# Performance work log

Hardware: AMD Instinct MI355X
Metric: run time of the kernel (lower is better)

## Reference

```python
import jax, jax.numpy as jnp
import numpy as np


def setup_inputs() -> dict:
    key = jax.random.key(0)
    inputs = jax.random.normal(key, (32, 56, 56, 256), dtype=jnp.float32)
    return {"inputs": inputs, "n": 48}


def reference(inputs, n):
    # Flatten per batch row: [B, H*W*C]
    B = inputs.shape[0]
    flat = inputs.reshape(B, -1)
    # k-th largest value per row is the threshold
    values, _ = jax.lax.top_k(flat, n)
    thresholds = values[:, -1].reshape(B, 1, 1, 1)
    mask = (inputs >= thresholds).astype(inputs.dtype)
    return inputs * mask
```

## Files before the change

### kernel.cpp

```cpp
#include <hip/hip_runtime.h>
#include <stdint.h>

#define ROWS 32
#define ROW_LEN 802816
#define ROW_LEN4 200704
#define BPR 98
#define F4_PER_BLOCK 2048
#define THREADS 256
#define F4_PER_THREAD 8
#define TG 3.0f
#define BCAP 40
#define CAP_ROW (BPR * BCAP)
#define SLOTS_PT 16

#define OFF_BCNT 501760
#define OFF_THR  514304

__device__ __forceinline__ uint32_t fkey(float x) {
    uint32_t u = __float_as_uint(x);
    return (u & 0x80000000u) ? ~u : (u | 0x80000000u);
}
__device__ __forceinline__ float fkey_inv(uint32_t k) {
    uint32_t u = (k & 0x80000000u) ? (k & 0x7FFFFFFFu) : ~k;
    return __uint_as_float(u);
}

__global__ __launch_bounds__(THREADS) void k_spec(const float* __restrict__ in,
                                                  uint32_t* __restrict__ cand,
                                                  int* __restrict__ bcnt) {
    __shared__ uint32_t lc[BCAP];
    __shared__ int lcnt;
    const int row = blockIdx.x / BPR;
    const int blk = blockIdx.x % BPR;
    if (threadIdx.x == 0) lcnt = 0;
    __syncthreads();
    const float4* p = (const float4*)in + (size_t)row * ROW_LEN4
                      + (size_t)blk * F4_PER_BLOCK + threadIdx.x;
#pragma unroll
    for (int v = 0; v < F4_PER_THREAD; ++v) {
        float4 d = p[v * THREADS];
        if (d.x > TG) { int q = atomicAdd(&lcnt, 1); if (q < BCAP) lc[q] = fkey(d.x); }
        if (d.y > TG) { int q = atomicAdd(&lcnt, 1); if (q < BCAP) lc[q] = fkey(d.y); }
        if (d.z > TG) { int q = atomicAdd(&lcnt, 1); if (q < BCAP) lc[q] = fkey(d.z); }
        if (d.w > TG) { int q = atomicAdd(&lcnt, 1); if (q < BCAP) lc[q] = fkey(d.w); }
    }
    __syncthreads();
    const int c = lcnt;
    if (threadIdx.x == 0) bcnt[row * BPR + blk] = c;
    const int cc = c < BCAP ? c : BCAP;
    for (int i = threadIdx.x; i < cc; i += THREADS)
        cand[((size_t)row * BPR + blk) * BCAP + i] = lc[i];
}

__device__ __forceinline__ void pick_digit(uint32_t* h, int t, int r,
                                           int* sh_sel, int* sh_rank) {
#pragma unroll
    for (int off = 1; off < 256; off <<= 1) {
        uint32_t v = h[t] + ((t + off < 256) ? h[t + off] : 0u);
        __syncthreads();
        h[t] = v;
        __syncthreads();
    }
    const uint32_t Sd = h[t];
    const uint32_t Sd1 = (t < 255) ? h[t + 1] : 0u;
    if ((int)Sd >= r && (int)Sd1 < r) { *sh_sel = t; *sh_rank = r - (int)Sd1; }
    __syncthreads();
}

__global__ __launch_bounds__(THREADS) void k_sel(const float* __restrict__ in,
                                                 const int* __restrict__ n_ptr,
                                                 const int* __restrict__ bcnt,
                                                 const uint32_t* __restrict__ cand,
                                                 float* __restrict__ thr) {
    __shared__ int lb[BPR];
    __shared__ uint32_t h[256];
    __shared__ int sh_sel, sh_rank, sh_m, sh_bad;
    const int row = blockIdx.x;
    const int t = threadIdx.x;
    const int n = *n_ptr;

    if (t == 0) { sh_m = 0; sh_bad = 0; }
    __syncthreads();
    {
        int lsum = 0, lbad = 0;
        for (int b = t; b < BPR; b += THREADS) {
            const int c = bcnt[row * BPR + b];
            lbad |= (c > BCAP);
            const int cc = c < BCAP ? c : BCAP;
            lb[b] = cc;
            lsum += cc;
        }
        if (lsum) atomicAdd(&sh_m, lsum);
        if (lbad) atomicOr(&sh_bad, 1);
    }
    __syncthreads();
    const int m = sh_m;
    const bool ok = (!sh_bad) && (m >= n) && (n >= 1);

    if (ok) {
        uint32_t key[SLOTS_PT];
        bool val[SLOTS_PT];
#pragma unroll
        for (int j = 0; j < SLOTS_PT; ++j) {
            const int slot = j * THREADS + t;
            uint32_t k = 0; bool v = false;
            if (slot < CAP_ROW) {
                k = cand[(size_t)row * CAP_ROW + slot];
                const int b = slot / BCAP;
                v = (slot - b * BCAP) < lb[b];
            }
            key[j] = k; val[j] = v;
        }
        uint32_t prefix = 0, msk = 0;
        int r = n;
        for (int rd = 0; rd < 4; ++rd) {
            const int shn = 24 - rd * 8;
            h[t] = 0;
            __syncthreads();
#pragma unroll
            for (int j = 0; j < SLOTS_PT; ++j)
                if (val[j] && (key[j] & msk) == prefix)
                    atomicAdd(&h[(key[j] >> shn) & 255u], 1u);
            __syncthreads();
            pick_digit(h, t, r, &sh_sel, &sh_rank);
            prefix |= ((uint32_t)sh_sel) << shn;
            msk |= 255u << shn;
            r = sh_rank;
            __syncthreads();
        }
        if (t == 0) thr[row] = fkey_inv(prefix);
    } else {
        uint32_t prefix = 0, msk = 0;
        int r = (n < 1) ? 1 : n;
        const float4* p = (const float4*)in + (size_t)row * ROW_LEN4;
        for (int rd = 0; rd < 4; ++rd) {
            const int shn = 24 - rd * 8;
            h[t] = 0;
            __syncthreads();
            for (int i = t; i < ROW_LEN4; i += THREADS) {
                const float4 d = p[i];
                uint32_t k;
                k = fkey(d.x); if ((k & msk) == prefix) atomicAdd(&h[(k >> shn) & 255u], 1u);
                k = fkey(d.y); if ((k & msk) == prefix) atomicAdd(&h[(k >> shn) & 255u], 1u);
                k = fkey(d.z); if ((k & msk) == prefix) atomicAdd(&h[(k >> shn) & 255u], 1u);
                k = fkey(d.w); if ((k & msk) == prefix) atomicAdd(&h[(k >> shn) & 255u], 1u);
            }
            __syncthreads();
            pick_digit(h, t, r, &sh_sel, &sh_rank);
            prefix |= ((uint32_t)sh_sel) << shn;
            msk |= 255u << shn;
            r = sh_rank;
            __syncthreads();
        }
        if (t == 0) thr[row] = fkey_inv(prefix);
    }
}

__global__ __launch_bounds__(THREADS) void k_mask(const float* __restrict__ in,
                                                  const float* __restrict__ thr,
                                                  float* __restrict__ out) {
    const int row = blockIdx.x / BPR;
    const int blk = blockIdx.x % BPR;
    const float t = thr[row];
    const size_t base = (size_t)row * ROW_LEN4 + (size_t)blk * F4_PER_BLOCK + threadIdx.x;
    const float4* p = (const float4*)in + base;
    float4* q = (float4*)out + base;
#pragma unroll
    for (int v = 0; v < F4_PER_THREAD; ++v) {
        float4 d = p[v * THREADS];
        d.x = (d.x >= t) ? d.x : 0.0f;
        d.y = (d.y >= t) ? d.y : 0.0f;
        d.z = (d.z >= t) ? d.z : 0.0f;
        d.w = (d.w >= t) ? d.w : 0.0f;
        q[v * THREADS] = d;
    }
}

extern "C" void kernel_launch(void* const* d_in, const int* in_sizes, int n_in,
                              void* d_out, int out_size, void* d_ws, size_t ws_size,
                              hipStream_t stream) {
    const float* in = (const float*)d_in[0];
    const int* n_ptr = (const int*)d_in[1];
    float* out = (float*)d_out;
    char* ws = (char*)d_ws;

    uint32_t* cand = (uint32_t*)ws;
    int* bcnt = (int*)(ws + OFF_BCNT);
    float* thr = (float*)(ws + OFF_THR);

    k_spec<<<ROWS * BPR, THREADS, 0, stream>>>(in, cand, bcnt);
    k_sel<<<ROWS, THREADS, 0, stream>>>(in, n_ptr, bcnt, cand, thr);
    k_mask<<<ROWS * BPR, THREADS, 0, stream>>>(in, thr, out);
}
```

Measured before the change: 55.05 us.

## Replace full masking pass with output memset plus sparse scatter of survivors

Removes the separate masking kernel, which read the whole input again and wrote the whole output. The output is now cleared with an async memset. The speculative pass records the positions of candidates instead of their keys, and the selection kernel gathers their values, finds the threshold, and writes only the surviving elements into the zeroed output. This removes one full read of the input, at the cost of an extra memset launch. The rare fallback path now does the masking itself with only one block per row, which would be slow when it runs.

```diff
diff --git a/kernel.cpp b/kernel.cpp
--- a/kernel.cpp
+++ b/kernel.cpp
@@ -26,9 +26,9 @@
 }
 
 __global__ __launch_bounds__(THREADS) void k_spec(const float* __restrict__ in,
-                                                  uint32_t* __restrict__ cand,
+                                                  uint32_t* __restrict__ pos,
                                                   int* __restrict__ bcnt) {
-    __shared__ uint32_t lc[BCAP];
+    __shared__ uint32_t lp[BCAP];
     __shared__ int lcnt;
     const int row = blockIdx.x / BPR;
     const int blk = blockIdx.x % BPR;
@@ -39,17 +39,18 @@
 #pragma unroll
     for (int v = 0; v < F4_PER_THREAD; ++v) {
         float4 d = p[v * THREADS];
-        if (d.x > TG) { int q = atomicAdd(&lcnt, 1); if (q < BCAP) lc[q] = fkey(d.x); }
-        if (d.y > TG) { int q = atomicAdd(&lcnt, 1); if (q < BCAP) lc[q] = fkey(d.y); }
-        if (d.z > TG) { int q = atomicAdd(&lcnt, 1); if (q < BCAP) lc[q] = fkey(d.z); }
-        if (d.w > TG) { int q = atomicAdd(&lcnt, 1); if (q < BCAP) lc[q] = fkey(d.w); }
+        const uint32_t e = (uint32_t)(blk * F4_PER_BLOCK + v * THREADS + threadIdx.x) * 4u;
+        if (d.x > TG) { int q = atomicAdd(&lcnt, 1); if (q < BCAP) lp[q] = e + 0u; }
+        if (d.y > TG) { int q = atomicAdd(&lcnt, 1); if (q < BCAP) lp[q] = e + 1u; }
+        if (d.z > TG) { int q = atomicAdd(&lcnt, 1); if (q < BCAP) lp[q] = e + 2u; }
+        if (d.w > TG) { int q = atomicAdd(&lcnt, 1); if (q < BCAP) lp[q] = e + 3u; }
     }
     __syncthreads();
     const int c = lcnt;
     if (threadIdx.x == 0) bcnt[row * BPR + blk] = c;
     const int cc = c < BCAP ? c : BCAP;
     for (int i = threadIdx.x; i < cc; i += THREADS)
-        cand[((size_t)row * BPR + blk) * BCAP + i] = lc[i];
+        pos[((size_t)row * BPR + blk) * BCAP + i] = lp[i];
 }
 
 __device__ __forceinline__ void pick_digit(uint32_t* h, int t, int r,
@@ -70,7 +71,8 @@
 __global__ __launch_bounds__(THREADS) void k_sel(const float* __restrict__ in,
                                                  const int* __restrict__ n_ptr,
                                                  const int* __restrict__ bcnt,
-                                                 const uint32_t* __restrict__ cand,
+                                                 const uint32_t* __restrict__ pos,
+                                                 float* __restrict__ out,
                                                  float* __restrict__ thr) {
     __shared__ int lb[BPR];
     __shared__ uint32_t h[256];
@@ -78,6 +80,8 @@
     const int row = blockIdx.x;
     const int t = threadIdx.x;
     const int n = *n_ptr;
+    const float* rin = in + (size_t)row * ROW_LEN;
+    float* rout = out + (size_t)row * ROW_LEN;
 
     if (t == 0) { sh_m = 0; sh_bad = 0; }
     __syncthreads();
@@ -99,17 +103,21 @@
 
     if (ok) {
         uint32_t key[SLOTS_PT];
+        uint32_t ps[SLOTS_PT];
         bool val[SLOTS_PT];
 #pragma unroll
         for (int j = 0; j < SLOTS_PT; ++j) {
             const int slot = j * THREADS + t;
-            uint32_t k = 0; bool v = false;
+            uint32_t k = 0, pp = 0; bool v = false;
             if (slot < CAP_ROW) {
-                k = cand[(size_t)row * CAP_ROW + slot];
                 const int b = slot / BCAP;
                 v = (slot - b * BCAP) < lb[b];
+                if (v) {
+                    pp = pos[(size_t)row * CAP_ROW + slot];
+                    k = fkey(rin[pp]);
+                }
             }
-            key[j] = k; val[j] = v;
+            key[j] = k; ps[j] = pp; val[j] = v;
         }
         uint32_t prefix = 0, msk = 0;
         int r = n;
@@ -128,11 +136,15 @@
             r = sh_rank;
             __syncthreads();
         }
+#pragma unroll
+        for (int j = 0; j < SLOTS_PT; ++j)
+            if (val[j] && key[j] >= prefix)
+                rout[ps[j]] = fkey_inv(key[j]);
         if (t == 0) thr[row] = fkey_inv(prefix);
     } else {
         uint32_t prefix = 0, msk = 0;
         int r = (n < 1) ? 1 : n;
-        const float4* p = (const float4*)in + (size_t)row * ROW_LEN4;
+        const float4* p = (const float4*)rin;
         for (int rd = 0; rd < 4; ++rd) {
             const int shn = 24 - rd * 8;
             h[t] = 0;
@@ -152,27 +164,17 @@
             r = sh_rank;
             __syncthreads();
         }
-        if (t == 0) thr[row] = fkey_inv(prefix);
-    }
-}
-
-__global__ __launch_bounds__(THREADS) void k_mask(const float* __restrict__ in,
-                                                  const float* __restrict__ thr,
-                                                  float* __restrict__ out) {
-    const int row = blockIdx.x / BPR;
-    const int blk = blockIdx.x % BPR;
-    const float t = thr[row];
-    const size_t base = (size_t)row * ROW_LEN4 + (size_t)blk * F4_PER_BLOCK + threadIdx.x;
-    const float4* p = (const float4*)in + base;
-    float4* q = (float4*)out + base;
-#pragma unroll
-    for (int v = 0; v < F4_PER_THREAD; ++v) {
-        float4 d = p[v * THREADS];
-        d.x = (d.x >= t) ? d.x : 0.0f;
-        d.y = (d.y >= t) ? d.y : 0.0f;
-        d.z = (d.z >= t) ? d.z : 0.0f;
-        d.w = (d.w >= t) ? d.w : 0.0f;
-        q[v * THREADS] = d;
+        const float tf = fkey_inv(prefix);
+        float4* q = (float4*)rout;
+        for (int i = t; i < ROW_LEN4; i += THREADS) {
+            float4 d = p[i];
+            d.x = (d.x >= tf) ? d.x : 0.0f;
+            d.y = (d.y >= tf) ? d.y : 0.0f;
+            d.z = (d.z >= tf) ? d.z : 0.0f;
+            d.w = (d.w >= tf) ? d.w : 0.0f;
+            q[i] = d;
+        }
+        if (t == 0) thr[row] = tf;
     }
 }
 
@@ -184,11 +186,11 @@
     float* out = (float*)d_out;
     char* ws = (char*)d_ws;
 
-    uint32_t* cand = (uint32_t*)ws;
+    uint32_t* pos = (uint32_t*)ws;
     int* bcnt = (int*)(ws + OFF_BCNT);
     float* thr = (float*)(ws + OFF_THR);
 
-    k_spec<<<ROWS * BPR, THREADS, 0, stream>>>(in, cand, bcnt);
-    k_sel<<<ROWS, THREADS, 0, stream>>>(in, n_ptr, bcnt, cand, thr);
-    k_mask<<<ROWS * BPR, THREADS, 0, stream>>>(in, thr, out);
+    hipMemsetAsync(out, 0, (size_t)out_size * sizeof(float), stream);
+    k_spec<<<ROWS * BPR, THREADS, 0, stream>>>(in, pos, bcnt);
+    k_sel<<<ROWS, THREADS, 0, stream>>>(in, n_ptr, bcnt, pos, out, thr);
 }
```

Result: no change. 54.46 us (-1.1%).

## Store candidate positions and replace mask pass with zero-fill plus scatter

Applied to the files above, without the earlier changes.

The speculative pass now records element positions rather than keys, batches all loads up front, and skips the atomic path for whole wavefronts with no value above the guess. When the fast path succeeded, the final kernel writes zeros and scatters only the surviving candidates instead of re-reading the full input. This removes a second full read of the input at the cost of a flag and a dependent gather in the select and scatter kernels. The zero-fill and scatter in the same block rely on a block barrier to order the writes.

```diff
diff --git a/kernel.cpp b/kernel.cpp
--- a/kernel.cpp
+++ b/kernel.cpp
@@ -15,6 +15,7 @@
 
 #define OFF_BCNT 501760
 #define OFF_THR  514304
+#define OFF_FLAG 514432
 
 __device__ __forceinline__ uint32_t fkey(float x) {
     uint32_t u = __float_as_uint(x);
@@ -28,7 +29,7 @@
 __global__ __launch_bounds__(THREADS) void k_spec(const float* __restrict__ in,
                                                   uint32_t* __restrict__ cand,
                                                   int* __restrict__ bcnt) {
-    __shared__ uint32_t lc[BCAP];
+    __shared__ uint32_t lp[BCAP];
     __shared__ int lcnt;
     const int row = blockIdx.x / BPR;
     const int blk = blockIdx.x % BPR;
@@ -36,20 +37,26 @@
     __syncthreads();
     const float4* p = (const float4*)in + (size_t)row * ROW_LEN4
                       + (size_t)blk * F4_PER_BLOCK + threadIdx.x;
+    float4 d[F4_PER_THREAD];
+#pragma unroll
+    for (int v = 0; v < F4_PER_THREAD; ++v) d[v] = p[v * THREADS];
 #pragma unroll
     for (int v = 0; v < F4_PER_THREAD; ++v) {
-        float4 d = p[v * THREADS];
-        if (d.x > TG) { int q = atomicAdd(&lcnt, 1); if (q < BCAP) lc[q] = fkey(d.x); }
-        if (d.y > TG) { int q = atomicAdd(&lcnt, 1); if (q < BCAP) lc[q] = fkey(d.y); }
-        if (d.z > TG) { int q = atomicAdd(&lcnt, 1); if (q < BCAP) lc[q] = fkey(d.z); }
-        if (d.w > TG) { int q = atomicAdd(&lcnt, 1); if (q < BCAP) lc[q] = fkey(d.w); }
+        const float mx = fmaxf(fmaxf(d[v].x, d[v].y), fmaxf(d[v].z, d[v].w));
+        if (__any(mx > TG)) {
+            const uint32_t e = (uint32_t)(blk * F4_PER_BLOCK + v * THREADS + threadIdx.x) * 4u;
+            if (d[v].x > TG) { int j = atomicAdd(&lcnt, 1); if (j < BCAP) lp[j] = e + 0u; }
+            if (d[v].y > TG) { int j = atomicAdd(&lcnt, 1); if (j < BCAP) lp[j] = e + 1u; }
+            if (d[v].z > TG) { int j = atomicAdd(&lcnt, 1); if (j < BCAP) lp[j] = e + 2u; }
+            if (d[v].w > TG) { int j = atomicAdd(&lcnt, 1); if (j < BCAP) lp[j] = e + 3u; }
+        }
     }
     __syncthreads();
     const int c = lcnt;
     if (threadIdx.x == 0) bcnt[row * BPR + blk] = c;
     const int cc = c < BCAP ? c : BCAP;
     for (int i = threadIdx.x; i < cc; i += THREADS)
-        cand[((size_t)row * BPR + blk) * BCAP + i] = lc[i];
+        cand[((size_t)row * BPR + blk) * BCAP + i] = lp[i];
 }
 
 __device__ __forceinline__ void pick_digit(uint32_t* h, int t, int r,
@@ -71,13 +78,15 @@
                                                  const int* __restrict__ n_ptr,
                                                  const int* __restrict__ bcnt,
                                                  const uint32_t* __restrict__ cand,
-                                                 float* __restrict__ thr) {
+                                                 float* __restrict__ thr,
+                                                 int* __restrict__ flag) {
     __shared__ int lb[BPR];
     __shared__ uint32_t h[256];
     __shared__ int sh_sel, sh_rank, sh_m, sh_bad;
     const int row = blockIdx.x;
     const int t = threadIdx.x;
     const int n = *n_ptr;
+    const float* rin = in + (size_t)row * ROW_LEN;
 
     if (t == 0) { sh_m = 0; sh_bad = 0; }
     __syncthreads();
@@ -105,9 +114,9 @@
             const int slot = j * THREADS + t;
             uint32_t k = 0; bool v = false;
             if (slot < CAP_ROW) {
-                k = cand[(size_t)row * CAP_ROW + slot];
                 const int b = slot / BCAP;
                 v = (slot - b * BCAP) < lb[b];
+                if (v) k = fkey(rin[cand[(size_t)row * CAP_ROW + slot]]);
             }
             key[j] = k; val[j] = v;
         }
@@ -128,11 +137,11 @@
             r = sh_rank;
             __syncthreads();
         }
-        if (t == 0) thr[row] = fkey_inv(prefix);
+        if (t == 0) { thr[row] = fkey_inv(prefix); flag[row] = 1; }
     } else {
         uint32_t prefix = 0, msk = 0;
         int r = (n < 1) ? 1 : n;
-        const float4* p = (const float4*)in + (size_t)row * ROW_LEN4;
+        const float4* p = (const float4*)rin;
         for (int rd = 0; rd < 4; ++rd) {
             const int shn = 24 - rd * 8;
             h[t] = 0;
@@ -152,27 +161,47 @@
             r = sh_rank;
             __syncthreads();
         }
-        if (t == 0) thr[row] = fkey_inv(prefix);
-    }
-}
-
-__global__ __launch_bounds__(THREADS) void k_mask(const float* __restrict__ in,
-                                                  const float* __restrict__ thr,
-                                                  float* __restrict__ out) {
+        if (t == 0) { thr[row] = fkey_inv(prefix); flag[row] = 0; }
+    }
+}
+
+__global__ __launch_bounds__(THREADS) void k_fillscatter(const float* __restrict__ in,
+                                                         const int* __restrict__ bcnt,
+                                                         const uint32_t* __restrict__ cand,
+                                                         const float* __restrict__ thr,
+                                                         const int* __restrict__ flag,
+                                                         float* __restrict__ out) {
     const int row = blockIdx.x / BPR;
     const int blk = blockIdx.x % BPR;
-    const float t = thr[row];
+    const float tf = thr[row];
     const size_t base = (size_t)row * ROW_LEN4 + (size_t)blk * F4_PER_BLOCK + threadIdx.x;
-    const float4* p = (const float4*)in + base;
     float4* q = (float4*)out + base;
-#pragma unroll
-    for (int v = 0; v < F4_PER_THREAD; ++v) {
-        float4 d = p[v * THREADS];
-        d.x = (d.x >= t) ? d.x : 0.0f;
-        d.y = (d.y >= t) ? d.y : 0.0f;
-        d.z = (d.z >= t) ? d.z : 0.0f;
-        d.w = (d.w >= t) ? d.w : 0.0f;
-        q[v * THREADS] = d;
+    if (flag[row]) {
+        const float4 z = make_float4(0.f, 0.f, 0.f, 0.f);
+#pragma unroll
+        for (int v = 0; v < F4_PER_THREAD; ++v)
+            q[v * THREADS] = z;
+        const int c0 = bcnt[row * BPR + blk];
+        const int c = c0 < BCAP ? c0 : BCAP;
+        __syncthreads();
+        const float* rin = in + (size_t)row * ROW_LEN;
+        float* rout = out + (size_t)row * ROW_LEN;
+        for (int i = threadIdx.x; i < c; i += THREADS) {
+            const uint32_t pos = cand[((size_t)row * BPR + blk) * BCAP + i];
+            const float v = rin[pos];
+            if (v >= tf) rout[pos] = v;
+        }
+    } else {
+        const float4* p = (const float4*)in + base;
+#pragma unroll
+        for (int v = 0; v < F4_PER_THREAD; ++v) {
+            float4 d = p[v * THREADS];
+            d.x = (d.x >= tf) ? d.x : 0.0f;
+            d.y = (d.y >= tf) ? d.y : 0.0f;
+            d.z = (d.z >= tf) ? d.z : 0.0f;
+            d.w = (d.w >= tf) ? d.w : 0.0f;
+            q[v * THREADS] = d;
+        }
     }
 }
 
@@ -187,8 +216,9 @@
     uint32_t* cand = (uint32_t*)ws;
     int* bcnt = (int*)(ws + OFF_BCNT);
     float* thr = (float*)(ws + OFF_THR);
+    int* flag = (int*)(ws + OFF_FLAG);
 
     k_spec<<<ROWS * BPR, THREADS, 0, stream>>>(in, cand, bcnt);
-    k_sel<<<ROWS, THREADS, 0, stream>>>(in, n_ptr, bcnt, cand, thr);
-    k_mask<<<ROWS * BPR, THREADS, 0, stream>>>(in, thr, out);
-}
+    k_sel<<<ROWS, THREADS, 0, stream>>>(in, n_ptr, bcnt, cand, thr, flag);
+    k_fillscatter<<<ROWS * BPR, THREADS, 0, stream>>>(in, bcnt, cand, thr, flag, out);
+}
```

Result: no change. 54.81 us (-0.4%).
